# Kernel optimization log

Hardware: AMD Instinct MI355X
Metric: run time of the kernel (lower is better)

## Reference

```python
import jax, jax.numpy as jnp
import numpy as np

B, D, LD, LP = 8, 192, 128, 1024
FC = [1024, 1024, 512]
NC = 2


def setup_inputs() -> dict:
    key = jax.random.key(0)
    ks = jax.random.split(key, 18)
    s = 0.05  # small init scale for numerical sanity
    inp = {
        "drug_conv": jax.random.normal(ks[0], (B, D, LD), jnp.float32),
        "protein_conv": jax.random.normal(ks[1], (B, D, LP), jnp.float32),
        "Wd": jax.random.normal(ks[2], (D, D), jnp.float32) * s,
        "bd": jax.random.normal(ks[3], (D,), jnp.float32) * s,
        "Wp": jax.random.normal(ks[4], (D, D), jnp.float32) * s,
        "bp": jax.random.normal(ks[5], (D,), jnp.float32) * s,
        "Wa": jax.random.normal(ks[6], (D, D), jnp.float32) * s,
        "ba": jax.random.normal(ks[7], (D,), jnp.float32) * s,
        "W1": jax.random.normal(ks[8], (FC[0], 2 * D), jnp.float32) * s,
        "b1": jax.random.normal(ks[9], (FC[0],), jnp.float32) * s,
        "W2": jax.random.normal(ks[10], (FC[1], FC[0]), jnp.float32) * s,
        "b2": jax.random.normal(ks[11], (FC[1],), jnp.float32) * s,
        "W3": jax.random.normal(ks[12], (FC[2], FC[1]), jnp.float32) * s,
        "b3": jax.random.normal(ks[13], (FC[2],), jnp.float32) * s,
        "Wo": jax.random.normal(ks[14], (NC, FC[2]), jnp.float32) * s,
        "bo": jax.random.normal(ks[15], (NC,), jnp.float32) * s,
    }
    return inp


def reference(drug_conv, protein_conv, Wd, bd, Wp, bp, Wa, ba,
              W1, b1, W2, b2, W3, b3, Wo, bo):
    # drug_conv: (B, D, Ld); protein_conv: (B, D, Lp). Torch Linear: y = x @ W.T + b
    d_att = jnp.einsum('bdl,ed->ble', drug_conv, Wd) + bd      # (B, Ld, D)
    p_att = jnp.einsum('bdl,ed->ble', protein_conv, Wp) + bp   # (B, Lp, D)
    # broadcast additive cross-attention: (B, Ld, Lp, D)
    h = jax.nn.relu(d_att[:, :, None, :] + p_att[:, None, :, :])
    A = jnp.einsum('blpd,ed->blpe', h, Wa) + ba                # (B, Ld, Lp, D)
    comp_att = jax.nn.sigmoid(jnp.mean(A, axis=2))             # (B, Ld, D)
    prot_att = jax.nn.sigmoid(jnp.mean(A, axis=1))             # (B, Lp, D)
    # gated residual: x*0.5 + x*att  (att permuted back to (B, D, L))
    drug = drug_conv * (0.5 + jnp.transpose(comp_att, (0, 2, 1)))
    prot = protein_conv * (0.5 + jnp.transpose(prot_att, (0, 2, 1)))
    # MaxPool1d over full sequence length == max along last axis
    drug_pooled = jnp.max(drug, axis=2)                        # (B, D)
    prot_pooled = jnp.max(prot, axis=2)                        # (B, D)
    pair = jnp.concatenate([drug_pooled, prot_pooled], axis=1) # (B, 2D)
    lrelu = lambda x: jax.nn.leaky_relu(x, 0.01)
    h1 = lrelu(pair @ W1.T + b1)
    h2 = lrelu(h1 @ W2.T + b2)
    h3 = lrelu(h2 @ W3.T + b3)
    return h3 @ Wo.T + bo                                      # (B, num_classes)
```

## Files before the change

### kernel.cpp

```cpp
#include <hip/hip_runtime.h>
#include <math.h>

#define BB 8
#define DD 192
#define LLD 128
#define LLP 1024
#define FC1 1024
#define FC2 1024
#define FC3 512
#define NCLS 2
#define LT 8

__device__ __forceinline__ void atomicMaxFloat(float* addr, float value) {
    if (value >= 0.f)
        atomicMax((int*)addr, __float_as_int(value));
    else
        atomicMin((unsigned int*)addr, __float_as_uint(value));
}

__global__ void proj_both_kernel(const float* __restrict__ drug,
                                 const float* __restrict__ prot,
                                 const float* __restrict__ Wd,
                                 const float* __restrict__ bdv,
                                 const float* __restrict__ Wp,
                                 const float* __restrict__ bpv,
                                 float* __restrict__ d_att,
                                 float* __restrict__ p_att) {
    int blk = blockIdx.x;
    const float *x, *W, *bias;
    float* y;
    int L, b, l0;
    if (blk < BB * (LLD / LT)) {
        x = drug; W = Wd; bias = bdv; y = d_att; L = LLD;
        b = blk >> 4; l0 = (blk & 15) * LT;
    } else {
        int idx = blk - BB * (LLD / LT);
        x = prot; W = Wp; bias = bpv; y = p_att; L = LLP;
        b = idx >> 7; l0 = (idx & 127) * LT;
    }
    int tid = threadIdx.x;

    __shared__ float xs[LT][DD + 4];

    const float* xbase = x + (size_t)b * DD * L + l0;
#pragma unroll
    for (int k = 0; k < LT; ++k) {
        int idx = tid + k * DD;
        int d = idx >> 3;
        int j = idx & (LT - 1);
        xs[j][d] = xbase[(size_t)d * L + j];
    }
    __syncthreads();

    const int e = tid;
    const float be = bias[e];
    float acc[LT];
#pragma unroll
    for (int j = 0; j < LT; ++j) acc[j] = be;

    const float4* Wr4 = (const float4*)(W + (size_t)e * DD);
#pragma unroll 2
    for (int d4 = 0; d4 < DD / 4; ++d4) {
        float4 w = Wr4[d4];
#pragma unroll
        for (int j = 0; j < LT; ++j) {
            float4 h = *(const float4*)&xs[j][d4 * 4];
            acc[j] = fmaf(h.x, w.x, acc[j]);
            acc[j] = fmaf(h.y, w.y, acc[j]);
            acc[j] = fmaf(h.z, w.z, acc[j]);
            acc[j] = fmaf(h.w, w.w, acc[j]);
        }
    }

    float* ybase = y + ((size_t)b * L + l0) * DD;
#pragma unroll
    for (int j = 0; j < LT; ++j)
        ybase[(size_t)j * DD + e] = acc[j];
}

__global__ void cross_sort_kernel(const float* __restrict__ da,
                                  const float* __restrict__ pa,
                                  float* __restrict__ Hd_t,
                                  float* __restrict__ Hp_t,
                                  float* __restrict__ pair) {
    int blk = blockIdx.x;
    int b = blk / (DD / 2);
    int dp = blk - b * (DD / 2);
    int d0 = dp * 2;
    int tid = threadIdx.x;

    __shared__ float skey[2][LLD];
    __shared__ int   sidx[2][LLD];
    __shared__ float sufs[2][LLD + 1];
    __shared__ int   cnt[2][LLD + 1];
    __shared__ float val[2][LLD + 1];

    if (tid < 4) {
        int side = tid >> 1;
        int dd = d0 + (tid & 1);
        pair[b * 2 * DD + side * DD + dd] = -INFINITY;
    }

    {
        int a = tid >> 7, l = tid & 127;
        skey[a][l] = da[((size_t)b * LLD + l) * DD + d0 + a];
        sidx[a][l] = l;
    }
    for (int i = tid; i < 2 * (LLD + 1); i += 256) {
        int a = i / (LLD + 1), k = i - a * (LLD + 1);
        cnt[a][k] = 0;
        val[a][k] = 0.f;
    }
    if (tid < 2) sufs[tid][LLD] = 0.f;
    __syncthreads();

    {
        int a = tid >> 7, i = tid & 127;
        for (int k = 2; k <= LLD; k <<= 1) {
            for (int j = k >> 1; j > 0; j >>= 1) {
                int ixj = i ^ j;
                if (ixj > i) {
                    float ki = skey[a][i], kj = skey[a][ixj];
                    bool up = ((i & k) == 0);
                    if ((ki > kj) == up) {
                        skey[a][i] = kj; skey[a][ixj] = ki;
                        int t = sidx[a][i]; sidx[a][i] = sidx[a][ixj]; sidx[a][ixj] = t;
                    }
                }
                __syncthreads();
            }
        }
    }

    {
        int a = tid >> 7, i = tid & 127;
        sufs[a][i] = skey[a][i];
        __syncthreads();
        for (int off = 1; off < LLD; off <<= 1) {
            float v = (i + off < LLD) ? sufs[a][i + off] : 0.f;
            __syncthreads();
            sufs[a][i] += v;
            __syncthreads();
        }
    }

    {
        int d_i = tid & 1, prow = tid >> 1;
        float* hprow = Hp_t + ((size_t)b * DD + d0 + d_i) * LLP;
        const float* qbase = pa + (size_t)b * LLP * DD + d0 + d_i;
#pragma unroll
        for (int batch = 0; batch < LLP / 128; ++batch) {
            int p = batch * 128 + prow;
            float q = qbase[(size_t)p * DD];
            float nq = -q;
            int pos = 0;
#pragma unroll
            for (int st = LLD; st > 0; st >>= 1) {
                int np = pos + st;
                if (np <= LLD && skey[d_i][np - 1] <= nq) pos = np;
            }
            hprow[p] = ((float)(LLD - pos) * q + sufs[d_i][pos]) * (1.0f / LLD);
            atomicAdd(&cnt[d_i][pos], 1);
            atomicAdd(&val[d_i][pos], q);
        }
    }
    __syncthreads();

    {
        int a = tid >> 7, i = tid & 127;
        for (int off = 1; off < LLD; off <<= 1) {
            int c = 0; float v = 0.f;
            if (i >= off) { c = cnt[a][i - off]; v = val[a][i - off]; }
            __syncthreads();
            cnt[a][i] += c;
            val[a][i] += v;
            __syncthreads();
        }
    }

    {
        int a = tid >> 7, r = tid & 127;
        float hv = (skey[a][r] * (float)cnt[a][r] + val[a][r]) * (1.0f / LLP);
        Hd_t[((size_t)b * DD + d0 + a) * LLD + sidx[a][r]] = hv;
    }
}

__global__ void gemm_sig_pool_kernel(const float* __restrict__ Hd_t,
                                     const float* __restrict__ Hp_t,
                                     const float* __restrict__ Wa,
                                     const float* __restrict__ ba,
                                     const float* __restrict__ drug,
                                     const float* __restrict__ prot,
                                     float* __restrict__ pair) {
    int blk = blockIdx.x;
    const float* Ht;
    const float* xsrc;
    int L, b, l0, side;
    if (blk < BB * (LLD / LT)) {
        b = blk >> 4; l0 = (blk & 15) * LT;
        Ht = Hd_t; xsrc = drug; L = LLD; side = 0;
    } else {
        int idx = blk - BB * (LLD / LT);
        b = idx >> 7; l0 = (idx & 127) * LT;
        Ht = Hp_t; xsrc = prot; L = LLP; side = 1;
    }
    int tid = threadIdx.x;

    __shared__ float hs[LT][DD + 4];

    const float* hrow = Ht + ((size_t)b * DD + tid) * L + l0;
#pragma unroll
    for (int j = 0; j < LT; ++j) hs[j][tid] = hrow[j];
    __syncthreads();

    const int e = tid;
    const float bias = ba[e];
    float acc[LT];
#pragma unroll
    for (int j = 0; j < LT; ++j) acc[j] = bias;

    const float4* Wr4 = (const float4*)(Wa + (size_t)e * DD);
#pragma unroll 2
    for (int d4 = 0; d4 < DD / 4; ++d4) {
        float4 w = Wr4[d4];
#pragma unroll
        for (int j = 0; j < LT; ++j) {
            float4 h = *(const float4*)&hs[j][d4 * 4];
            acc[j] = fmaf(h.x, w.x, acc[j]);
            acc[j] = fmaf(h.y, w.y, acc[j]);
            acc[j] = fmaf(h.z, w.z, acc[j]);
            acc[j] = fmaf(h.w, w.w, acc[j]);
        }
    }

    const float* xrow = xsrc + ((size_t)b * DD + e) * L + l0;
    float4 x0 = *(const float4*)&xrow[0];
    float4 x1 = *(const float4*)&xrow[4];
    float xv[LT] = {x0.x, x0.y, x0.z, x0.w, x1.x, x1.y, x1.z, x1.w};
    float m = -INFINITY;
#pragma unroll
    for (int j = 0; j < LT; ++j) {
        float gate = 0.5f + 1.0f / (1.0f + __expf(-acc[j]));
        m = fmaxf(m, xv[j] * gate);
    }
    atomicMaxFloat(&pair[b * 2 * DD + side * DD + e], m);
}

__global__ void fc_wave_kernel(const float* __restrict__ x,
                               const float* __restrict__ W,
                               const float* __restrict__ bias,
                               float* __restrict__ y,
                               int K, int N, int leaky) {
    int gtid = blockIdx.x * blockDim.x + threadIdx.x;
    int wid = gtid >> 6;
    int lane = gtid & 63;
    if (wid >= BB * N) return;
    int b = wid / N;
    int j = wid - b * N;
    const float4* xr = (const float4*)(x + (size_t)b * K);
    const float4* Wr = (const float4*)(W + (size_t)j * K);
    int K4 = K >> 2;
    float s = 0.f;
    for (int k = lane; k < K4; k += 64) {
        float4 xv = xr[k];
        float4 wv = Wr[k];
        s = fmaf(xv.x, wv.x, s);
        s = fmaf(xv.y, wv.y, s);
        s = fmaf(xv.z, wv.z, s);
        s = fmaf(xv.w, wv.w, s);
    }
#pragma unroll
    for (int off = 32; off > 0; off >>= 1) s += __shfl_xor(s, off);
    if (lane == 0) {
        float acc = s + bias[j];
        if (leaky) acc = (acc > 0.f) ? acc : 0.01f * acc;
        y[wid] = acc;
    }
}

extern "C" void kernel_launch(void* const* d_in, const int* in_sizes, int n_in,
                              void* d_out, int out_size, void* d_ws, size_t ws_size,
                              hipStream_t stream) {
    const float* drug = (const float*)d_in[0];
    const float* prot = (const float*)d_in[1];
    const float* Wd = (const float*)d_in[2];
    const float* bd = (const float*)d_in[3];
    const float* Wp = (const float*)d_in[4];
    const float* bp = (const float*)d_in[5];
    const float* Wa = (const float*)d_in[6];
    const float* ba = (const float*)d_in[7];
    const float* W1 = (const float*)d_in[8];
    const float* b1 = (const float*)d_in[9];
    const float* W2 = (const float*)d_in[10];
    const float* b2 = (const float*)d_in[11];
    const float* W3 = (const float*)d_in[12];
    const float* b3 = (const float*)d_in[13];
    const float* Wo = (const float*)d_in[14];
    const float* bo = (const float*)d_in[15];
    float* out = (float*)d_out;

    float* ws = (float*)d_ws;
    const size_t n_datt = (size_t)BB * LLD * DD;
    const size_t n_patt = (size_t)BB * LLP * DD;
    float* d_att  = ws;
    float* p_att  = d_att + n_datt;
    float* Hd_t   = p_att + n_patt;
    float* Hp_t   = Hd_t + n_datt;
    float* pair   = Hp_t + n_patt;
    float* h1     = pair + (size_t)BB * 2 * DD;
    float* h2     = h1 + (size_t)BB * FC1;
    float* h3     = h2 + (size_t)BB * FC2;

    proj_both_kernel<<<BB * (LLD / LT) + BB * (LLP / LT), DD, 0, stream>>>(
        drug, prot, Wd, bd, Wp, bp, d_att, p_att);

    cross_sort_kernel<<<BB * (DD / 2), 256, 0, stream>>>(d_att, p_att, Hd_t, Hp_t, pair);

    gemm_sig_pool_kernel<<<BB * (LLD / LT) + BB * (LLP / LT), DD, 0, stream>>>(
        Hd_t, Hp_t, Wa, ba, drug, prot, pair);

    fc_wave_kernel<<<(BB * FC1 * 64) / 256, 256, 0, stream>>>(pair, W1, b1, h1, 2 * DD, FC1, 1);
    fc_wave_kernel<<<(BB * FC2 * 64) / 256, 256, 0, stream>>>(h1, W2, b2, h2, FC1, FC2, 1);
    fc_wave_kernel<<<(BB * FC3 * 64) / 256, 256, 0, stream>>>(h2, W3, b3, h3, FC2, FC3, 1);
    fc_wave_kernel<<<(BB * NCLS * 64 + 255) / 256, 256, 0, stream>>>(h3, Wo, bo, out, FC3, NCLS, 0);
}
```

Measured before the change: 94.50 us.

## Sort and scan per wave in registers with shuffles instead of shared-memory barriers

```diff
diff --git a/kernel.cpp b/kernel.cpp
--- a/kernel.cpp
+++ b/kernel.cpp
@@ -88,61 +88,81 @@
     int dp = blk - b * (DD / 2);
     int d0 = dp * 2;
     int tid = threadIdx.x;
+    int wave = tid >> 6, lane = tid & 63;
 
     __shared__ float skey[2][LLD];
-    __shared__ int   sidx[2][LLD];
     __shared__ float sufs[2][LLD + 1];
     __shared__ int   cnt[2][LLD + 1];
     __shared__ float val[2][LLD + 1];
 
-    if (tid < 4) {
-        int side = tid >> 1;
-        int dd = d0 + (tid & 1);
-        pair[b * 2 * DD + side * DD + dd] = -INFINITY;
-    }
-
-    {
-        int a = tid >> 7, l = tid & 127;
-        skey[a][l] = da[((size_t)b * LLD + l) * DD + d0 + a];
-        sidx[a][l] = l;
-    }
-    for (int i = tid; i < 2 * (LLD + 1); i += 256) {
-        int a = i / (LLD + 1), k = i - a * (LLD + 1);
-        cnt[a][k] = 0;
-        val[a][k] = 0.f;
-    }
-    if (tid < 2) sufs[tid][LLD] = 0.f;
-    __syncthreads();
-
-    {
-        int a = tid >> 7, i = tid & 127;
+    float s0 = 0.f, s1 = 0.f;
+    int i0 = 0, i1 = 0;
+
+    if (wave < 2) {
+        const int a = wave;
+        const float* base = da + (size_t)b * LLD * DD + d0 + a;
+        s0 = base[(size_t)lane * DD];
+        s1 = base[(size_t)(lane + 64) * DD];
+        i0 = lane; i1 = lane + 64;
+
         for (int k = 2; k <= LLD; k <<= 1) {
             for (int j = k >> 1; j > 0; j >>= 1) {
-                int ixj = i ^ j;
-                if (ixj > i) {
-                    float ki = skey[a][i], kj = skey[a][ixj];
-                    bool up = ((i & k) == 0);
-                    if ((ki > kj) == up) {
-                        skey[a][i] = kj; skey[a][ixj] = ki;
-                        int t = sidx[a][i]; sidx[a][i] = sidx[a][ixj]; sidx[a][ixj] = t;
+                if (j == 64) {
+                    if (s0 > s1) {
+                        float tk = s0; s0 = s1; s1 = tk;
+                        int ti = i0; i0 = i1; i1 = ti;
+                    }
+                } else {
+                    {
+                        float pk = __shfl_xor(s0, j);
+                        int   pi = __shfl_xor(i0, j);
+                        bool keep_min = (((lane & k) == 0) == ((lane & j) == 0));
+                        bool take = keep_min ? (pk < s0) : (pk > s0);
+                        if (take) { s0 = pk; i0 = pi; }
+                    }
+                    {
+                        int e = lane | 64;
+                        float pk = __shfl_xor(s1, j);
+                        int   pi = __shfl_xor(i1, j);
+                        bool keep_min = (((e & k) == 0) == ((e & j) == 0));
+                        bool take = keep_min ? (pk < s1) : (pk > s1);
+                        if (take) { s1 = pk; i1 = pi; }
                     }
                 }
-                __syncthreads();
             }
         }
-    }
-
-    {
-        int a = tid >> 7, i = tid & 127;
-        sufs[a][i] = skey[a][i];
-        __syncthreads();
-        for (int off = 1; off < LLD; off <<= 1) {
-            float v = (i + off < LLD) ? sufs[a][i + off] : 0.f;
-            __syncthreads();
-            sufs[a][i] += v;
-            __syncthreads();
-        }
-    }
+
+        float t1 = s1;
+#pragma unroll
+        for (int off = 1; off < 64; off <<= 1) {
+            int src = lane + off;
+            float v = __shfl(t1, src & 63);
+            t1 += (src < 64) ? v : 0.f;
+        }
+        float tot1 = __shfl(t1, 0);
+        float t0 = s0;
+#pragma unroll
+        for (int off = 1; off < 64; off <<= 1) {
+            int src = lane + off;
+            float v = __shfl(t0, src & 63);
+            t0 += (src < 64) ? v : 0.f;
+        }
+
+        skey[a][lane] = s0;
+        skey[a][lane + 64] = s1;
+        sufs[a][lane] = t0 + tot1;
+        sufs[a][lane + 64] = t1;
+        if (lane == 0) sufs[a][LLD] = 0.f;
+    } else if (wave == 2) {
+        for (int i = lane; i < 2 * (LLD + 1); i += 64) ((int*)cnt)[i] = 0;
+        if (lane < 4) {
+            int side = lane >> 1;
+            pair[b * 2 * DD + side * DD + d0 + (lane & 1)] = -INFINITY;
+        }
+    } else {
+        for (int i = lane; i < 2 * (LLD + 1); i += 64) ((float*)val)[i] = 0.f;
+    }
+    __syncthreads();
 
     {
         int d_i = tid & 1, prow = tid >> 1;
@@ -166,22 +186,31 @@
     }
     __syncthreads();
 
-    {
-        int a = tid >> 7, i = tid & 127;
-        for (int off = 1; off < LLD; off <<= 1) {
-            int c = 0; float v = 0.f;
-            if (i >= off) { c = cnt[a][i - off]; v = val[a][i - off]; }
-            __syncthreads();
-            cnt[a][i] += c;
-            val[a][i] += v;
-            __syncthreads();
-        }
-    }
-
-    {
-        int a = tid >> 7, r = tid & 127;
-        float hv = (skey[a][r] * (float)cnt[a][r] + val[a][r]) * (1.0f / LLP);
-        Hd_t[((size_t)b * DD + d0 + a) * LLD + sidx[a][r]] = hv;
+    if (wave < 2) {
+        const int a = wave;
+        int   c0 = cnt[a][lane], c1 = cnt[a][lane + 64];
+        float v0 = val[a][lane], v1 = val[a][lane + 64];
+#pragma unroll
+        for (int off = 1; off < 64; off <<= 1) {
+            int src = lane - off;
+            int   cu = __shfl(c0, src & 63);
+            float vu = __shfl(v0, src & 63);
+            if (src >= 0) { c0 += cu; v0 += vu; }
+        }
+        int   ct0 = __shfl(c0, 63);
+        float vt0 = __shfl(v0, 63);
+#pragma unroll
+        for (int off = 1; off < 64; off <<= 1) {
+            int src = lane - off;
+            int   cu = __shfl(c1, src & 63);
+            float vu = __shfl(v1, src & 63);
+            if (src >= 0) { c1 += cu; v1 += vu; }
+        }
+        c1 += ct0; v1 += vt0;
+
+        float* hdrow = Hd_t + ((size_t)b * DD + d0 + a) * LLD;
+        hdrow[i0] = (s0 * (float)c0 + v0) * (1.0f / LLP);
+        hdrow[i1] = (s1 * (float)c1 + v1) * (1.0f / LLP);
     }
 }
 
```

Result: no change. 94.60 us (+0.1%).
